# Kernel optimization log

Hardware: AMD Instinct MI355X
Metric: run time of the kernel (lower is better)

Reference implementation:

```python
import jax, jax.numpy as jnp
import numpy as np

B, V, E, D_IN, D_OUT = 8, 10000, 160000, 128, 128
BN_EPS = 1e-5


def setup_inputs() -> dict:
    key = jax.random.key(0)
    ks = jax.random.split(key, 8)
    X = jax.random.normal(ks[0], (B, V, D_IN), dtype=jnp.float32)
    edge_attr = jax.random.normal(ks[1], (B, E), dtype=jnp.float32)
    W_node = jax.random.normal(ks[2], (D_OUT, D_IN), dtype=jnp.float32) * (1.0 / np.sqrt(D_IN))
    W_edge = jax.random.normal(ks[3], (D_OUT, 1), dtype=jnp.float32)
    W_self = jax.random.normal(ks[4], (D_OUT, D_IN), dtype=jnp.float32) * (1.0 / np.sqrt(D_IN))
    b_self = jax.random.normal(ks[5], (D_OUT,), dtype=jnp.float32) * 0.01
    gamma = jnp.ones((D_OUT,), dtype=jnp.float32)
    beta = jnp.zeros((D_OUT,), dtype=jnp.float32)
    edge_index = jax.random.randint(ks[6], (E, 2), 0, V, dtype=jnp.int32)
    return {"X": X, "edge_attr": edge_attr, "W_node": W_node, "W_edge": W_edge,
            "W_self": W_self, "b_self": b_self, "gamma": gamma, "beta": beta,
            "edge_index": edge_index}


def reference(X, edge_attr, W_node, W_edge, W_self, b_self, gamma, beta, edge_index):
    src = edge_index[:, 0]  # [E]
    dst = edge_index[:, 1]  # [E]
    # self-loop linear
    H = jnp.einsum('bvf,of->bvo', X, W_self) + b_self  # [B,V,D_OUT]
    # fused gather -> per-edge message -> scatter-add
    msg = jnp.einsum('bef,of->beo', X[:, src, :], W_node)  # [B,E,D_OUT]
    msg = msg + edge_attr[:, :, None] * W_edge[:, 0][None, None, :]
    aggregated = jnp.zeros_like(H).at[:, dst, :].add(msg)
    H = H + aggregated
    # BatchNorm1d over channel dim (training mode, biased variance over B*V)
    mean = jnp.mean(H, axis=(0, 1))
    var = jnp.var(H, axis=(0, 1))
    Hn = (H - mean) * jax.lax.rsqrt(var + BN_EPS) * gamma + beta
    return jax.nn.relu(Hn)
```

## Files before the change

kernel.cpp:

```cpp
#include <hip/hip_runtime.h>

#define B_ 8
#define V_ 10000
#define E_ 160000
#define DIN 128
#define DOUT 128
#define M_ (B_*V_)
#define NINV (1.0f/80000.0f)
#define BN_EPS 1e-5f

#define GEMM_BLOCKS 625

#define WS_COUNTS  0
#define WS_SCL     10000
#define WS_SHF     10128
#define WS_ROWPTR  10512
#define WS_CURSOR  20513
#define WS_SSRC    30513
#define WS_EAS     190520
#define WS_S       1470520
#define WS_WPK     1550520
#define WS_XH      1566904
#define WS_AH      6686904
#define WS_PART    11806904
#define WS_ZERO_UNITS 10000

typedef __attribute__((ext_vector_type(2))) _Float16 half2_t;
typedef __attribute__((ext_vector_type(4))) _Float16 half4_t;
typedef __attribute__((ext_vector_type(8))) _Float16 half8_t;
typedef __attribute__((ext_vector_type(4))) float f32x4;

__device__ inline half2_t i2h(unsigned i) {
    half2_t h; __builtin_memcpy(&h, &i, 4); return h;
}
__device__ inline unsigned h2i(half2_t h) {
    unsigned i; __builtin_memcpy(&i, &h, 4); return i;
}

__global__ __launch_bounds__(256) void prep_kernel(
    const float* __restrict__ X, _Float16* __restrict__ Xh,
    const float* __restrict__ Wself, const float* __restrict__ Wnode,
    _Float16* __restrict__ Wpk,
    const int* __restrict__ EI, int* __restrict__ counts)
{
    const int blk = blockIdx.x;
    const int t = threadIdx.x;
    if (blk < 10000) {
        int idx = blk * 256 + t;
        float4 v = ((const float4*)X)[idx];
        half4_t o = { (_Float16)v.x, (_Float16)v.y, (_Float16)v.z, (_Float16)v.w };
        ((half4_t*)Xh)[idx] = o;
    } else if (blk < 10016) {
        int g = (blk - 10000) * 256 + t;
        int pair = g >> 6;
        int lane = g & 63;
        int ks = pair >> 3;
        int nt = pair & 7;
        int o = nt * 16 + (lane & 15);
        int k = ks * 32 + (lane >> 4) * 8;
        const float* wsrc = (k < 128) ? (Wself + o * 128 + k)
                                      : (Wnode + o * 128 + (k - 128));
        _Float16* dst = Wpk + ((size_t)pair * 64 + lane) * 8;
#pragma unroll
        for (int j = 0; j < 8; ++j) dst[j] = (_Float16)wsrc[j];
    } else {
        int e = (blk - 10016) * 256 + t;
        if (e < E_) atomicAdd(&counts[EI[2 * e + 1]], 1);
    }
}

__global__ __launch_bounds__(256) void scan_kernel(
    const int* __restrict__ counts, int* __restrict__ row_ptr,
    int* __restrict__ cursor)
{
    __shared__ int psum[256];
    const int t = threadIdx.x;
    const int base = t * 40;
    int local[40];
    int s = 0;
#pragma unroll
    for (int i = 0; i < 40; ++i) {
        int idx = base + i;
        int c = (idx < V_) ? counts[idx] : 0;
        local[i] = s;
        s += c;
    }
    psum[t] = s;
    __syncthreads();
    for (int off = 1; off < 256; off <<= 1) {
        int v = (t >= off) ? psum[t - off] : 0;
        __syncthreads();
        psum[t] += v;
        __syncthreads();
    }
    int excl = (t == 0) ? 0 : psum[t - 1];
#pragma unroll
    for (int i = 0; i < 40; ++i) {
        int idx = base + i;
        if (idx < V_) {
            int rp = excl + local[i];
            row_ptr[idx] = rp;
            cursor[idx] = rp;
        }
    }
    if (t == 255) row_ptr[V_] = psum[255];
}

__global__ __launch_bounds__(256) void bucket_kernel(
    const int* __restrict__ EI, const float* __restrict__ EA,
    int* __restrict__ cursor, int* __restrict__ ssrc,
    float* __restrict__ EAs)
{
    int e = blockIdx.x * 256 + threadIdx.x;
    if (e < E_) {
        int src = EI[2 * e];
        int dst = EI[2 * e + 1];
        int p = atomicAdd(&cursor[dst], 1);
        ssrc[p] = src;
        float4 v0, v1;
        v0.x = EA[0 * E_ + e]; v0.y = EA[1 * E_ + e];
        v0.z = EA[2 * E_ + e]; v0.w = EA[3 * E_ + e];
        v1.x = EA[4 * E_ + e]; v1.y = EA[5 * E_ + e];
        v1.z = EA[6 * E_ + e]; v1.w = EA[7 * E_ + e];
        *(float4*)(EAs + (size_t)p * 8) = v0;
        *(float4*)(EAs + (size_t)p * 8 + 4) = v1;
    }
}

__global__ __launch_bounds__(256) void gather_kernel(
    const _Float16* __restrict__ Xh, const float* __restrict__ EAs,
    const int* __restrict__ row_ptr, const int* __restrict__ ssrc,
    _Float16* __restrict__ Ah, float* __restrict__ S)
{
    const int b = blockIdx.x & 7;
    const int dblk = blockIdx.x >> 3;
    const int w = threadIdx.x >> 6;
    const int lane = threadIdx.x & 63;
    const int q = lane >> 4;
    const int sl = lane & 15;
    const int d = dblk * 4 + w;
    const int wid = b * V_ + d;
    const int k0 = row_ptr[d];
    const int k1 = row_ptr[d + 1];
    const _Float16* Xb = Xh + (size_t)b * V_ * DIN + sl * 8;
    half2_t a0 = (half2_t)0, a1 = (half2_t)0, a2 = (half2_t)0, a3 = (half2_t)0;
    float ea = 0.0f;
    for (int kb = k0; kb < k1; kb += 64) {
        int cnt = min(64, k1 - kb);
        int msrc = 0;
        if (lane < cnt) {
            msrc = ssrc[kb + lane];
            ea += EAs[(size_t)(kb + lane) * 8 + b];
        }
        int j = 0;
        for (; j + 16 <= cnt; j += 16) {
#pragma unroll
            for (int u = 0; u < 4; ++u) {
                int s = __shfl(msrc, j + u * 4 + q);
                uint4 v = *(const uint4*)(Xb + (size_t)s * DIN);
                a0 += i2h(v.x); a1 += i2h(v.y); a2 += i2h(v.z); a3 += i2h(v.w);
            }
        }
        for (; j + 4 <= cnt; j += 4) {
            int s = __shfl(msrc, j + q);
            uint4 v = *(const uint4*)(Xb + (size_t)s * DIN);
            a0 += i2h(v.x); a1 += i2h(v.y); a2 += i2h(v.z); a3 += i2h(v.w);
        }
        if (j < cnt) {
            int s = __shfl(msrc, j + q);
            if (j + q < cnt) {
                uint4 v = *(const uint4*)(Xb + (size_t)s * DIN);
                a0 += i2h(v.x); a1 += i2h(v.y); a2 += i2h(v.z); a3 += i2h(v.w);
            }
        }
    }
#pragma unroll
    for (int off = 32; off >= 16; off >>= 1) {
        a0 += i2h(__shfl_down(h2i(a0), off));
        a1 += i2h(__shfl_down(h2i(a1), off));
        a2 += i2h(__shfl_down(h2i(a2), off));
        a3 += i2h(__shfl_down(h2i(a3), off));
    }
    for (int off = 32; off; off >>= 1) ea += __shfl_down(ea, off);
    if (lane == 0) S[wid] = ea;
    if (lane < 16) {
        uint4 o;
        o.x = h2i(a0); o.y = h2i(a1); o.z = h2i(a2); o.w = h2i(a3);
        *(uint4*)(Ah + (size_t)wid * DIN + sl * 8) = o;
    }
}

template<bool STATS>
__device__ __forceinline__ void gemm_body(
    const _Float16* __restrict__ Xh, const _Float16* __restrict__ Ah,
    const _Float16* __restrict__ Wpk, const float* __restrict__ S,
    const float* __restrict__ bself, const float* __restrict__ wedge,
    int bid, int t, f32x4 (&acc)[2][8], float* cs, float* css,
    _Float16* wlds)
{
    const int wave = t >> 6;
    const int lane = t & 63;
    const int quad = lane >> 4;
    const int ln = lane & 15;
    const int rowbase = bid * 128 + wave * 32;
    const int m0 = rowbase + ln;
    const int m1 = rowbase + 16 + ln;

#pragma unroll
    for (int i = 0; i < 16; ++i) {
        int chunk = wave * 16 + i;
        __builtin_amdgcn_global_load_lds(
            (const __attribute__((address_space(1))) void*)
                ((const char*)Wpk + (size_t)chunk * 1024 + lane * 16),
            (__attribute__((address_space(3))) void*)
                ((char*)wlds + (size_t)chunk * 1024),
            16, 0, 0);
    }

    if constexpr (STATS) {
        if (t < 128) { cs[t] = 0.0f; css[t] = 0.0f; }
    }

#pragma unroll
    for (int mt = 0; mt < 2; ++mt)
#pragma unroll
        for (int nt = 0; nt < 8; ++nt) acc[mt][nt] = (f32x4){0.f, 0.f, 0.f, 0.f};

    const _Float16* X0 = Xh + (size_t)m0 * DIN + quad * 8;
    const _Float16* X1 = Xh + (size_t)m1 * DIN + quad * 8;
    const _Float16* A0 = Ah + (size_t)m0 * DIN + quad * 8;
    const _Float16* A1 = Ah + (size_t)m1 * DIN + quad * 8;

    half8_t afr[2][8];
#pragma unroll
    for (int ks = 0; ks < 4; ++ks) {
        afr[0][ks]     = *(const half8_t*)(X0 + ks * 32);
        afr[1][ks]     = *(const half8_t*)(X1 + ks * 32);
        afr[0][4 + ks] = *(const half8_t*)(A0 + ks * 32);
        afr[1][4 + ks] = *(const half8_t*)(A1 + ks * 32);
    }

    __syncthreads();

#pragma unroll
    for (int ks = 0; ks < 8; ++ks) {
#pragma unroll
        for (int nt = 0; nt < 8; ++nt) {
            half8_t bfr = *(const half8_t*)(wlds + (size_t)(ks * 8 + nt) * 512 + lane * 8);
            acc[0][nt] = __builtin_amdgcn_mfma_f32_16x16x32_f16(afr[0][ks], bfr, acc[0][nt], 0, 0, 0);
            acc[1][nt] = __builtin_amdgcn_mfma_f32_16x16x32_f16(afr[1][ks], bfr, acc[1][nt], 0, 0, 0);
        }
    }

    float bs[8], we[8];
#pragma unroll
    for (int nt = 0; nt < 8; ++nt) {
        int c = nt * 16 + ln;
        bs[nt] = bself[c];
        we[nt] = wedge[c];
    }
    float psum[8], psq[8];
    if constexpr (STATS) {
#pragma unroll
        for (int nt = 0; nt < 8; ++nt) { psum[nt] = 0.0f; psq[nt] = 0.0f; }
    }

#pragma unroll
    for (int mt = 0; mt < 2; ++mt) {
        const int rbase = rowbase + mt * 16 + quad * 4;
        float sv[4];
#pragma unroll
        for (int r = 0; r < 4; ++r) sv[r] = S[rbase + r];
#pragma unroll
        for (int nt = 0; nt < 8; ++nt) {
#pragma unroll
            for (int r = 0; r < 4; ++r) {
                float h = acc[mt][nt][r] + bs[nt] + sv[r] * we[nt];
                acc[mt][nt][r] = h;
                if constexpr (STATS) {
                    psum[nt] += h;
                    psq[nt] += h * h;
                }
            }
        }
    }
    if constexpr (STATS) {
#pragma unroll
        for (int nt = 0; nt < 8; ++nt) {
            psum[nt] += __shfl_down(psum[nt], 32);
            psum[nt] += __shfl_down(psum[nt], 16);
            psq[nt] += __shfl_down(psq[nt], 32);
            psq[nt] += __shfl_down(psq[nt], 16);
        }
        __syncthreads();
        if (lane < 16) {
#pragma unroll
            for (int nt = 0; nt < 8; ++nt) {
                atomicAdd(&cs[nt * 16 + ln], psum[nt]);
                atomicAdd(&css[nt * 16 + ln], psq[nt]);
            }
        }
        __syncthreads();
    }
}

__global__ __launch_bounds__(256) void stats_gemm_kernel(
    const _Float16* __restrict__ Xh, const _Float16* __restrict__ Ah,
    const _Float16* __restrict__ Wpk, const float* __restrict__ S,
    const float* __restrict__ bself, const float* __restrict__ wedge,
    float* __restrict__ Partials)
{
    __shared__ _Float16 wlds[32768];
    __shared__ float cs[128];
    __shared__ float css[128];
    const int t = threadIdx.x;
    f32x4 acc[2][8];
    gemm_body<true>(Xh, Ah, Wpk, S, bself, wedge, blockIdx.x, t, acc, cs, css,
                    wlds);
    Partials[(size_t)blockIdx.x * 256 + t] = (t < 128) ? cs[t] : css[t - 128];
}

__global__ __launch_bounds__(64) void finalize_stats_kernel(
    const float* __restrict__ Partials, const float* __restrict__ gamma,
    const float* __restrict__ beta, float* __restrict__ scl,
    float* __restrict__ shf)
{
    const int c = blockIdx.x;
    const int t = threadIdx.x;
    float s = 0.0f, q = 0.0f;
    for (int p = t; p < GEMM_BLOCKS; p += 64) {
        s += Partials[(size_t)p * 256 + c];
        q += Partials[(size_t)p * 256 + 128 + c];
    }
    for (int off = 32; off; off >>= 1) {
        s += __shfl_down(s, off);
        q += __shfl_down(q, off);
    }
    if (t == 0) {
        float mean = s * NINV;
        float rstd = rsqrtf(q * NINV - mean * mean + BN_EPS);
        float sc = gamma[c] * rstd;
        scl[c] = sc;
        shf[c] = beta[c] - mean * sc;
    }
}

__global__ __launch_bounds__(256) void norm_gemm_kernel(
    const _Float16* __restrict__ Xh, const _Float16* __restrict__ Ah,
    const _Float16* __restrict__ Wpk, const float* __restrict__ S,
    const float* __restrict__ bself, const float* __restrict__ wedge,
    const float* __restrict__ scl, const float* __restrict__ shf,
    float* __restrict__ H)
{
    __shared__ _Float16 wlds[32768];
    const int t = threadIdx.x;
    f32x4 acc[2][8];
    gemm_body<false>(Xh, Ah, Wpk, S, bself, wedge, blockIdx.x, t, acc,
                     nullptr, nullptr, wlds);

    const int wave = t >> 6;
    const int lane = t & 63;
    const int quad = lane >> 4;
    const int ln = lane & 15;
    const int rowbase = blockIdx.x * 128 + wave * 32;
    float sc[8], sh[8];
#pragma unroll
    for (int nt = 0; nt < 8; ++nt) {
        int c = nt * 16 + ln;
        sc[nt] = scl[c];
        sh[nt] = shf[c];
    }
#pragma unroll
    for (int mt = 0; mt < 2; ++mt) {
        const int rbase = rowbase + mt * 16 + quad * 4;
#pragma unroll
        for (int r = 0; r < 4; ++r) {
            float* Hr = H + (size_t)(rbase + r) * DOUT + ln;
#pragma unroll
            for (int nt = 0; nt < 8; ++nt)
                Hr[nt * 16] = fmaxf(acc[mt][nt][r] * sc[nt] + sh[nt], 0.0f);
        }
    }
}

extern "C" void kernel_launch(void* const* d_in, const int* in_sizes, int n_in,
                              void* d_out, int out_size, void* d_ws, size_t ws_size,
                              hipStream_t stream)
{
    const float* X      = (const float*)d_in[0];
    const float* EA     = (const float*)d_in[1];
    const float* Wnode  = (const float*)d_in[2];
    const float* Wedge  = (const float*)d_in[3];
    const float* Wself  = (const float*)d_in[4];
    const float* bself  = (const float*)d_in[5];
    const float* gamma  = (const float*)d_in[6];
    const float* beta   = (const float*)d_in[7];
    const int*   EI     = (const int*)d_in[8];

    int*   wsI    = (int*)d_ws;
    float* wsF    = (float*)d_ws;
    int*   counts = wsI + WS_COUNTS;
    float* scl    = wsF + WS_SCL;
    float* shf    = wsF + WS_SHF;
    int*   rowptr = wsI + WS_ROWPTR;
    int*   cursor = wsI + WS_CURSOR;
    int*   ssrc   = wsI + WS_SSRC;
    float* EAs    = wsF + WS_EAS;
    float* S      = wsF + WS_S;
    _Float16* Wpk = (_Float16*)(wsI + WS_WPK);
    _Float16* Xh  = (_Float16*)(wsI + WS_XH);
    _Float16* Ah  = (_Float16*)(wsI + WS_AH);
    float* Partials = wsF + WS_PART;
    float* H      = (float*)d_out;

    hipMemsetAsync(d_ws, 0, (size_t)WS_ZERO_UNITS * 4, stream);

    prep_kernel<<<10641, 256, 0, stream>>>(X, Xh, Wself, Wnode, Wpk, EI, counts);
    scan_kernel<<<1, 256, 0, stream>>>(counts, rowptr, cursor);
    bucket_kernel<<<(E_ + 255) / 256, 256, 0, stream>>>(EI, EA, cursor, ssrc, EAs);

    gather_kernel<<<M_ / 4, 256, 0, stream>>>(Xh, EAs, rowptr, ssrc, Ah, S);

    stats_gemm_kernel<<<GEMM_BLOCKS, 256, 0, stream>>>(Xh, Ah, Wpk, S, bself,
                                                       Wedge, Partials);
    finalize_stats_kernel<<<128, 64, 0, stream>>>(Partials, gamma, beta, scl, shf);
    norm_gemm_kernel<<<GEMM_BLOCKS, 256, 0, stream>>>(Xh, Ah, Wpk, S, bself,
                                                      Wedge, scl, shf, H);
}
```

Baseline: 218.7 us.

## Replace GEMM recompute with stored pre-norm output and elementwise norm pass

The GEMM previously ran twice, once to gather BatchNorm statistics and once to normalize. It now runs once, writing the pre-norm H to the output and accumulating per-channel sums into global memory with atomics, and a separate elementwise kernel then normalizes and applies ReLU in place. Edge-attribute sums are also moved out of the gather kernel: the bucket kernel adds them straight into S with atomics, which removes the EAs scratch buffer. This removes the second GEMM pass and the finalize kernel. In exchange it adds an extra 40MB read and write of H, more float atomics, and a memset that now covers S.

```diff
diff --git a/kernel.cpp b/kernel.cpp
--- a/kernel.cpp
+++ b/kernel.cpp
@@ -12,18 +12,16 @@
 #define GEMM_BLOCKS 625
 
 #define WS_COUNTS  0
-#define WS_SCL     10000
-#define WS_SHF     10128
-#define WS_ROWPTR  10512
-#define WS_CURSOR  20513
-#define WS_SSRC    30513
-#define WS_EAS     190520
-#define WS_S       1470520
-#define WS_WPK     1550520
-#define WS_XH      1566904
-#define WS_AH      6686904
-#define WS_PART    11806904
-#define WS_ZERO_UNITS 10000
+#define WS_SUM     10000
+#define WS_SUMSQ   10128
+#define WS_S       10256
+#define WS_ZERO_UNITS 90256
+#define WS_ROWPTR  90256
+#define WS_CURSOR  100257
+#define WS_SSRC    110257
+#define WS_WPK     270264
+#define WS_XH      286648
+#define WS_AH      5406648
 
 typedef __attribute__((ext_vector_type(2))) _Float16 half2_t;
 typedef __attribute__((ext_vector_type(4))) _Float16 half4_t;
@@ -109,7 +107,7 @@
 __global__ __launch_bounds__(256) void bucket_kernel(
     const int* __restrict__ EI, const float* __restrict__ EA,
     int* __restrict__ cursor, int* __restrict__ ssrc,
-    float* __restrict__ EAs)
+    float* __restrict__ S)
 {
     int e = blockIdx.x * 256 + threadIdx.x;
     if (e < E_) {
@@ -117,20 +115,16 @@
         int dst = EI[2 * e + 1];
         int p = atomicAdd(&cursor[dst], 1);
         ssrc[p] = src;
-        float4 v0, v1;
-        v0.x = EA[0 * E_ + e]; v0.y = EA[1 * E_ + e];
-        v0.z = EA[2 * E_ + e]; v0.w = EA[3 * E_ + e];
-        v1.x = EA[4 * E_ + e]; v1.y = EA[5 * E_ + e];
-        v1.z = EA[6 * E_ + e]; v1.w = EA[7 * E_ + e];
-        *(float4*)(EAs + (size_t)p * 8) = v0;
-        *(float4*)(EAs + (size_t)p * 8 + 4) = v1;
+#pragma unroll
+        for (int b = 0; b < 8; ++b)
+            atomicAdd(&S[b * V_ + dst], EA[(size_t)b * E_ + e]);
     }
 }
 
 __global__ __launch_bounds__(256) void gather_kernel(
-    const _Float16* __restrict__ Xh, const float* __restrict__ EAs,
+    const _Float16* __restrict__ Xh,
     const int* __restrict__ row_ptr, const int* __restrict__ ssrc,
-    _Float16* __restrict__ Ah, float* __restrict__ S)
+    _Float16* __restrict__ Ah)
 {
     const int b = blockIdx.x & 7;
     const int dblk = blockIdx.x >> 3;
@@ -144,14 +138,10 @@
     const int k1 = row_ptr[d + 1];
     const _Float16* Xb = Xh + (size_t)b * V_ * DIN + sl * 8;
     half2_t a0 = (half2_t)0, a1 = (half2_t)0, a2 = (half2_t)0, a3 = (half2_t)0;
-    float ea = 0.0f;
     for (int kb = k0; kb < k1; kb += 64) {
         int cnt = min(64, k1 - kb);
         int msrc = 0;
-        if (lane < cnt) {
-            msrc = ssrc[kb + lane];
-            ea += EAs[(size_t)(kb + lane) * 8 + b];
-        }
+        if (lane < cnt) msrc = ssrc[kb + lane];
         int j = 0;
         for (; j + 16 <= cnt; j += 16) {
 #pragma unroll
@@ -181,8 +171,6 @@
         a2 += i2h(__shfl_down(h2i(a2), off));
         a3 += i2h(__shfl_down(h2i(a3), off));
     }
-    for (int off = 32; off; off >>= 1) ea += __shfl_down(ea, off);
-    if (lane == 0) S[wid] = ea;
     if (lane < 16) {
         uint4 o;
         o.x = h2i(a0); o.y = h2i(a1); o.z = h2i(a2); o.w = h2i(a3);
@@ -190,19 +178,22 @@
     }
 }
 
-template<bool STATS>
-__device__ __forceinline__ void gemm_body(
+__global__ __launch_bounds__(256) void gemm_stats_kernel(
     const _Float16* __restrict__ Xh, const _Float16* __restrict__ Ah,
     const _Float16* __restrict__ Wpk, const float* __restrict__ S,
     const float* __restrict__ bself, const float* __restrict__ wedge,
-    int bid, int t, f32x4 (&acc)[2][8], float* cs, float* css,
-    _Float16* wlds)
-{
+    float* __restrict__ H, float* __restrict__ gsum,
+    float* __restrict__ gsumsq)
+{
+    __shared__ _Float16 wlds[32768];
+    __shared__ float cs[128];
+    __shared__ float css[128];
+    const int t = threadIdx.x;
     const int wave = t >> 6;
     const int lane = t & 63;
     const int quad = lane >> 4;
     const int ln = lane & 15;
-    const int rowbase = bid * 128 + wave * 32;
+    const int rowbase = blockIdx.x * 128 + wave * 32;
     const int m0 = rowbase + ln;
     const int m1 = rowbase + 16 + ln;
 
@@ -217,10 +208,9 @@
             16, 0, 0);
     }
 
-    if constexpr (STATS) {
-        if (t < 128) { cs[t] = 0.0f; css[t] = 0.0f; }
-    }
-
+    if (t < 128) { cs[t] = 0.0f; css[t] = 0.0f; }
+
+    f32x4 acc[2][8];
 #pragma unroll
     for (int mt = 0; mt < 2; ++mt)
 #pragma unroll
@@ -260,10 +250,8 @@
         we[nt] = wedge[c];
     }
     float psum[8], psq[8];
-    if constexpr (STATS) {
-#pragma unroll
-        for (int nt = 0; nt < 8; ++nt) { psum[nt] = 0.0f; psq[nt] = 0.0f; }
-    }
+#pragma unroll
+    for (int nt = 0; nt < 8; ++nt) { psum[nt] = 0.0f; psq[nt] = 0.0f; }
 
 #pragma unroll
     for (int mt = 0; mt < 2; ++mt) {
@@ -272,114 +260,67 @@
 #pragma unroll
         for (int r = 0; r < 4; ++r) sv[r] = S[rbase + r];
 #pragma unroll
-        for (int nt = 0; nt < 8; ++nt) {
-#pragma unroll
-            for (int r = 0; r < 4; ++r) {
-                float h = acc[mt][nt][r] + bs[nt] + sv[r] * we[nt];
-                acc[mt][nt][r] = h;
-                if constexpr (STATS) {
-                    psum[nt] += h;
-                    psq[nt] += h * h;
-                }
-            }
-        }
-    }
-    if constexpr (STATS) {
-#pragma unroll
-        for (int nt = 0; nt < 8; ++nt) {
-            psum[nt] += __shfl_down(psum[nt], 32);
-            psum[nt] += __shfl_down(psum[nt], 16);
-            psq[nt] += __shfl_down(psq[nt], 32);
-            psq[nt] += __shfl_down(psq[nt], 16);
-        }
-        __syncthreads();
-        if (lane < 16) {
-#pragma unroll
-            for (int nt = 0; nt < 8; ++nt) {
-                atomicAdd(&cs[nt * 16 + ln], psum[nt]);
-                atomicAdd(&css[nt * 16 + ln], psq[nt]);
-            }
-        }
-        __syncthreads();
-    }
-}
-
-__global__ __launch_bounds__(256) void stats_gemm_kernel(
-    const _Float16* __restrict__ Xh, const _Float16* __restrict__ Ah,
-    const _Float16* __restrict__ Wpk, const float* __restrict__ S,
-    const float* __restrict__ bself, const float* __restrict__ wedge,
-    float* __restrict__ Partials)
-{
-    __shared__ _Float16 wlds[32768];
-    __shared__ float cs[128];
-    __shared__ float css[128];
-    const int t = threadIdx.x;
-    f32x4 acc[2][8];
-    gemm_body<true>(Xh, Ah, Wpk, S, bself, wedge, blockIdx.x, t, acc, cs, css,
-                    wlds);
-    Partials[(size_t)blockIdx.x * 256 + t] = (t < 128) ? cs[t] : css[t - 128];
-}
-
-__global__ __launch_bounds__(64) void finalize_stats_kernel(
-    const float* __restrict__ Partials, const float* __restrict__ gamma,
-    const float* __restrict__ beta, float* __restrict__ scl,
-    float* __restrict__ shf)
-{
-    const int c = blockIdx.x;
-    const int t = threadIdx.x;
-    float s = 0.0f, q = 0.0f;
-    for (int p = t; p < GEMM_BLOCKS; p += 64) {
-        s += Partials[(size_t)p * 256 + c];
-        q += Partials[(size_t)p * 256 + 128 + c];
-    }
-    for (int off = 32; off; off >>= 1) {
-        s += __shfl_down(s, off);
-        q += __shfl_down(q, off);
-    }
-    if (t == 0) {
-        float mean = s * NINV;
-        float rstd = rsqrtf(q * NINV - mean * mean + BN_EPS);
-        float sc = gamma[c] * rstd;
-        scl[c] = sc;
-        shf[c] = beta[c] - mean * sc;
-    }
-}
-
-__global__ __launch_bounds__(256) void norm_gemm_kernel(
-    const _Float16* __restrict__ Xh, const _Float16* __restrict__ Ah,
-    const _Float16* __restrict__ Wpk, const float* __restrict__ S,
-    const float* __restrict__ bself, const float* __restrict__ wedge,
-    const float* __restrict__ scl, const float* __restrict__ shf,
-    float* __restrict__ H)
-{
-    __shared__ _Float16 wlds[32768];
-    const int t = threadIdx.x;
-    f32x4 acc[2][8];
-    gemm_body<false>(Xh, Ah, Wpk, S, bself, wedge, blockIdx.x, t, acc,
-                     nullptr, nullptr, wlds);
-
-    const int wave = t >> 6;
-    const int lane = t & 63;
-    const int quad = lane >> 4;
-    const int ln = lane & 15;
-    const int rowbase = blockIdx.x * 128 + wave * 32;
-    float sc[8], sh[8];
-#pragma unroll
-    for (int nt = 0; nt < 8; ++nt) {
-        int c = nt * 16 + ln;
-        sc[nt] = scl[c];
-        sh[nt] = shf[c];
-    }
-#pragma unroll
-    for (int mt = 0; mt < 2; ++mt) {
-        const int rbase = rowbase + mt * 16 + quad * 4;
-#pragma unroll
         for (int r = 0; r < 4; ++r) {
             float* Hr = H + (size_t)(rbase + r) * DOUT + ln;
 #pragma unroll
-            for (int nt = 0; nt < 8; ++nt)
-                Hr[nt * 16] = fmaxf(acc[mt][nt][r] * sc[nt] + sh[nt], 0.0f);
-        }
+            for (int nt = 0; nt < 8; ++nt) {
+                float h = acc[mt][nt][r] + bs[nt] + sv[r] * we[nt];
+                Hr[nt * 16] = h;
+                psum[nt] += h;
+                psq[nt] += h * h;
+            }
+        }
+    }
+#pragma unroll
+    for (int nt = 0; nt < 8; ++nt) {
+        psum[nt] += __shfl_down(psum[nt], 32);
+        psum[nt] += __shfl_down(psum[nt], 16);
+        psq[nt] += __shfl_down(psq[nt], 32);
+        psq[nt] += __shfl_down(psq[nt], 16);
+    }
+    __syncthreads();
+    if (lane < 16) {
+#pragma unroll
+        for (int nt = 0; nt < 8; ++nt) {
+            atomicAdd(&cs[nt * 16 + ln], psum[nt]);
+            atomicAdd(&css[nt * 16 + ln], psq[nt]);
+        }
+    }
+    __syncthreads();
+    if (t < 128) atomicAdd(&gsum[t], cs[t]);
+    else atomicAdd(&gsumsq[t - 128], css[t - 128]);
+}
+
+__global__ __launch_bounds__(256) void norm_relu_kernel(
+    float* __restrict__ H, const float* __restrict__ gsum,
+    const float* __restrict__ gsumsq, const float* __restrict__ gamma,
+    const float* __restrict__ beta)
+{
+    const int total = M_ * DOUT / 4;
+    for (int idx = blockIdx.x * 256 + threadIdx.x; idx < total;
+         idx += gridDim.x * 256) {
+        int o4 = (idx & 31) * 4;
+        float4 s = *(const float4*)(gsum + o4);
+        float4 q = *(const float4*)(gsumsq + o4);
+        float4 g = *(const float4*)(gamma + o4);
+        float4 bt = *(const float4*)(beta + o4);
+        float4 sc, sh;
+        {
+            float m0 = s.x * NINV, m1 = s.y * NINV, m2 = s.z * NINV, m3 = s.w * NINV;
+            float r0 = rsqrtf(q.x * NINV - m0 * m0 + BN_EPS);
+            float r1 = rsqrtf(q.y * NINV - m1 * m1 + BN_EPS);
+            float r2 = rsqrtf(q.z * NINV - m2 * m2 + BN_EPS);
+            float r3 = rsqrtf(q.w * NINV - m3 * m3 + BN_EPS);
+            sc.x = g.x * r0; sc.y = g.y * r1; sc.z = g.z * r2; sc.w = g.w * r3;
+            sh.x = bt.x - m0 * sc.x; sh.y = bt.y - m1 * sc.y;
+            sh.z = bt.z - m2 * sc.z; sh.w = bt.w - m3 * sc.w;
+        }
+        float4 h = ((const float4*)H)[idx];
+        h.x = fmaxf(h.x * sc.x + sh.x, 0.0f);
+        h.y = fmaxf(h.y * sc.y + sh.y, 0.0f);
+        h.z = fmaxf(h.z * sc.z + sh.z, 0.0f);
+        h.w = fmaxf(h.w * sc.w + sh.w, 0.0f);
+        ((float4*)H)[idx] = h;
     }
 }
 
@@ -400,30 +341,26 @@
     int*   wsI    = (int*)d_ws;
     float* wsF    = (float*)d_ws;
     int*   counts = wsI + WS_COUNTS;
-    float* scl    = wsF + WS_SCL;
-    float* shf    = wsF + WS_SHF;
+    float* gsum   = wsF + WS_SUM;
+    float* gsumsq = wsF + WS_SUMSQ;
+    float* S      = wsF + WS_S;
     int*   rowptr = wsI + WS_ROWPTR;
     int*   cursor = wsI + WS_CURSOR;
     int*   ssrc   = wsI + WS_SSRC;
-    float* EAs    = wsF + WS_EAS;
-    float* S      = wsF + WS_S;
     _Float16* Wpk = (_Float16*)(wsI + WS_WPK);
     _Float16* Xh  = (_Float16*)(wsI + WS_XH);
     _Float16* Ah  = (_Float16*)(wsI + WS_AH);
-    float* Partials = wsF + WS_PART;
     float* H      = (float*)d_out;
 
     hipMemsetAsync(d_ws, 0, (size_t)WS_ZERO_UNITS * 4, stream);
 
     prep_kernel<<<10641, 256, 0, stream>>>(X, Xh, Wself, Wnode, Wpk, EI, counts);
     scan_kernel<<<1, 256, 0, stream>>>(counts, rowptr, cursor);
-    bucket_kernel<<<(E_ + 255) / 256, 256, 0, stream>>>(EI, EA, cursor, ssrc, EAs);
-
-    gather_kernel<<<M_ / 4, 256, 0, stream>>>(Xh, EAs, rowptr, ssrc, Ah, S);
-
-    stats_gemm_kernel<<<GEMM_BLOCKS, 256, 0, stream>>>(Xh, Ah, Wpk, S, bself,
-                                                       Wedge, Partials);
-    finalize_stats_kernel<<<128, 64, 0, stream>>>(Partials, gamma, beta, scl, shf);
-    norm_gemm_kernel<<<GEMM_BLOCKS, 256, 0, stream>>>(Xh, Ah, Wpk, S, bself,
-                                                      Wedge, scl, shf, H);
-}
+    bucket_kernel<<<(E_ + 255) / 256, 256, 0, stream>>>(EI, EA, cursor, ssrc, S);
+
+    gather_kernel<<<M_ / 4, 256, 0, stream>>>(Xh, rowptr, ssrc, Ah);
+
+    gemm_stats_kernel<<<GEMM_BLOCKS, 256, 0, stream>>>(Xh, Ah, Wpk, S, bself,
+                                                       Wedge, H, gsum, gsumsq);
+    norm_relu_kernel<<<2048, 256, 0, stream>>>(H, gsum, gsumsq, gamma, beta);
+}
```

After: 276.0 us. 26.2% more time.
